# Kernel optimization log

Hardware: AMD Instinct MI355X
Metric: run time of the kernel (lower is better)

The kernel has to match this reference:

```python
import jax, jax.numpy as jnp
import numpy as np

L, D, H, B, SX, SY, VS, VT = 6, 1024, 16, 4, 512, 512, 32000, 32000
DK = D // H
FF = 4 * D
EPS = 1e-3          # LayerNorm eps (added to std, not var)
SCALE_EMB = float(np.sqrt(D))
NEG = -1e30         # stands in for -inf; fully-masked rows are zeroed after softmax


def pos_encoding(length, d):
    # tensor2tensor-style sinusoid: [sin | cos] concatenated along channels
    nt = d // 2
    lti = np.log(1e4) / (nt - 1)
    inv = np.exp(np.arange(nt) * -lti)
    st = np.arange(length)[:, None] * inv[None, :]
    return jnp.asarray(np.concatenate([np.sin(st), np.cos(st)], axis=1), jnp.float32)


def layer_norm(z, a, b):
    # faithful to the torch module: uses unbiased std (ddof=1) and divides by (std + eps)
    mu = z.mean(-1, keepdims=True)
    sig = jnp.sqrt(((z - mu) ** 2).sum(-1, keepdims=True) / (z.shape[-1] - 1))
    return (z - mu) / (sig + EPS) * a + b


def mha(xq, xkv, wq, wk, wv, wo, mask):
    # xq: (b, lq, D), xkv: (b, lk, D); head-chunking of channel dim == reshape to (H, DK)
    b, lq, _ = xq.shape
    q = (xq @ wq.T).reshape(b, lq, H, DK)
    k = (xkv @ wk.T).reshape(b, -1, H, DK)
    v = (xkv @ wv.T).reshape(b, -1, H, DK)
    s = jnp.einsum('bqhd,bkhd->bhqk', q, k) * (1.0 / np.sqrt(DK))
    m = mask[:, None, :, :]
    s = jnp.where(m, s, NEG)
    att = jax.nn.softmax(s, axis=-1)
    att = att * m.any(-1, keepdims=True)  # replicates NaN->0 for fully masked rows
    c = jnp.einsum('bhqk,bkhd->bqhd', att, v).reshape(b, lq, D)
    return c @ wo.T


def setup_inputs():
    key = jax.random.key(0)
    ks = jax.random.split(key, 10)
    s = 0.02
    emb_x = (jax.random.normal(ks[0], (VS, D), jnp.float32) * s).at[0].set(0.0)  # padding_idx=0
    emb_y = (jax.random.normal(ks[1], (VT, D), jnp.float32) * s).at[0].set(0.0)
    return {
        'emb_x': emb_x, 'emb_y': emb_y,
        'enc_qkvo': jax.random.normal(ks[2], (L, 4, D, D), jnp.float32) * s,
        'enc_ln_s': jnp.ones((L, 2, D), jnp.float32), 'enc_ln_b': jnp.zeros((L, 2, D), jnp.float32),
        'enc_w1': jax.random.normal(ks[3], (L, FF, D), jnp.float32) * s, 'enc_b1': jnp.zeros((L, FF), jnp.float32),
        'enc_w2': jax.random.normal(ks[4], (L, D, FF), jnp.float32) * s, 'enc_b2': jnp.zeros((L, D), jnp.float32),
        'dec_qkvo': jax.random.normal(ks[5], (L, 8, D, D), jnp.float32) * s,
        'dec_ln_s': jnp.ones((L, 3, D), jnp.float32), 'dec_ln_b': jnp.zeros((L, 3, D), jnp.float32),
        'dec_w1': jax.random.normal(ks[6], (L, FF, D), jnp.float32) * s, 'dec_b1': jnp.zeros((L, FF), jnp.float32),
        'dec_w2': jax.random.normal(ks[7], (L, D, FF), jnp.float32) * s, 'dec_b2': jnp.zeros((L, D), jnp.float32),
        'x_block': jax.random.randint(ks[8], (B, SX), 0, VS),
        'y_block': jax.random.randint(ks[9], (B, SY), 0, VT),
    }


def reference(emb_x, emb_y, enc_qkvo, enc_ln_s, enc_ln_b, enc_w1, enc_b1, enc_w2, enc_b2,
              dec_qkvo, dec_ln_s, dec_ln_b, dec_w1, dec_b1, dec_w2, dec_b2, x_block, y_block):
    # internal layout (b, len, D); torch code uses (b, D, len) -- math is identical
    ex = emb_x[x_block] * SCALE_EMB + pos_encoding(SX, D)[None]
    ey = emb_y[y_block] * SCALE_EMB + pos_encoding(SY, D)[None]
    xv = x_block != 0
    yv = y_block != 0
    xx = xv[:, :, None] & xv[:, None, :]                                   # (B, qx, kx)
    xy = yv[:, :, None] & xv[:, None, :]                                   # (B, qy, kx)
    yy = (yv[:, :, None] & yv[:, None, :]) & jnp.tril(jnp.ones((SY, SY), bool))[None]
    e = ex
    for i in range(L):
        sub = mha(e, e, enc_qkvo[i, 0], enc_qkvo[i, 1], enc_qkvo[i, 2], enc_qkvo[i, 3], xx)
        e = layer_norm(e + sub, enc_ln_s[i, 0], enc_ln_b[i, 0])
        sub = jax.nn.relu(e @ enc_w1[i].T + enc_b1[i]) @ enc_w2[i].T + enc_b2[i]
        e = layer_norm(e + sub, enc_ln_s[i, 1], enc_ln_b[i, 1])
    z = e
    e = ey
    for i in range(L):
        sub = mha(e, e, dec_qkvo[i, 0], dec_qkvo[i, 1], dec_qkvo[i, 2], dec_qkvo[i, 3], yy)
        e = layer_norm(e + sub, dec_ln_s[i, 0], dec_ln_b[i, 0])
        sub = mha(e, z, dec_qkvo[i, 4], dec_qkvo[i, 5], dec_qkvo[i, 6], dec_qkvo[i, 7], xy)
        e = layer_norm(e + sub, dec_ln_s[i, 1], dec_ln_b[i, 1])
        sub = jax.nn.relu(e @ dec_w1[i].T + dec_b1[i]) @ dec_w2[i].T + dec_b2[i]
        e = layer_norm(e + sub, dec_ln_s[i, 2], dec_ln_b[i, 2])
    return e @ emb_y.T  # tied output projection -> (B, SY, VT)
```

## Files before the change

### kernel.cpp

```cpp
#include <hip/hip_runtime.h>

typedef unsigned short u16;
typedef float f32x4 __attribute__((ext_vector_type(4)));
typedef __bf16 bf16x8 __attribute__((ext_vector_type(8)));
typedef u16 u16x8 __attribute__((ext_vector_type(8)));

#define DEV __device__ __forceinline__

DEV u16 f2bf(float f) {
  unsigned u = __builtin_bit_cast(unsigned, f);
  u += 0x7fffu + ((u >> 16) & 1u);
  return (u16)(u >> 16);
}

DEV float wsum(float v) {
#pragma unroll
  for (int o = 32; o > 0; o >>= 1) v += __shfl_xor(v, o, 64);
  return v;
}
DEV float gmax16(float v) {
#pragma unroll
  for (int o = 8; o > 0; o >>= 1) v = fmaxf(v, __shfl_xor(v, o, 64));
  return v;
}
DEV float gsum16(float v) {
#pragma unroll
  for (int o = 8; o > 0; o >>= 1) v += __shfl_xor(v, o, 64);
  return v;
}

DEV void gld16(const void* g, void* l) {
  __builtin_amdgcn_global_load_lds((const __attribute__((address_space(1))) void*)g,
                                   (__attribute__((address_space(3))) void*)l, 16, 0, 0);
}

template <int N>
DEV void vwait() {
  if constexpr (N == 0) asm volatile("s_waitcnt vmcnt(0)" ::: "memory");
  else if constexpr (N == 2) asm volatile("s_waitcnt vmcnt(2)" ::: "memory");
  else if constexpr (N == 4) asm volatile("s_waitcnt vmcnt(4)" ::: "memory");
  else asm volatile("s_waitcnt vmcnt(6)" ::: "memory");
}

DEV void remap_bxy(int& bx, int& by) {
  const int gx = gridDim.x, gy = gridDim.y;
  const int flat = blockIdx.y * gx + blockIdx.x;
  const int nwg = gx * gy;
  const int q = nwg >> 3, r = nwg & 7;
  const int xcd = flat & 7, li = flat >> 3;
  const int wg = (xcd < r ? xcd * (q + 1) : r * (q + 1) + (xcd - r) * q) + li;
  by = wg % gy;
  bx = wg / gy;
}

template <int BM, int BN, int MODE>
__global__ __launch_bounds__(256, 2) void gemm_k(
    const u16* __restrict__ A, const u16* __restrict__ B, int lda, int ldb, int K,
    float alpha, const float* __restrict__ bias, float* __restrict__ Cf, int ldc,
    u16* __restrict__ Cb, u16* __restrict__ qp, u16* __restrict__ kp,
    u16* __restrict__ vp, int n_off) {
  constexpr int FM = BM / 32, FN = BN / 32;
  constexpr int CHA = BM / 8, CHT = (BM + BN) / 8;
  __shared__ u16 lds[2][(BM + BN) * 64];
  const int lane = threadIdx.x & 63, wid = threadIdx.x >> 6;
  const int wr = wid >> 1, wc = wid & 1;
  int bx, by;
  remap_bxy(bx, by);
  const u16* gA = A + (long)(by * BM) * lda;
  const u16* gB = B + (long)(bx * BN) * ldb;

  const f32x4 zero4 = {0.f, 0.f, 0.f, 0.f};
  f32x4 acc[FM][FN];
#pragma unroll
  for (int m = 0; m < FM; ++m)
#pragma unroll
    for (int n = 0; n < FN; ++n) acc[m][n] = zero4;

  const int r8 = lane >> 3, sl = lane & 7;

  auto stage = [&](int buf, int kt) {
    const int kb = kt << 6;
#pragma unroll
    for (int c0 = 0; c0 < CHT; c0 += 4) {
      const int c = c0 + wid;
      u16* l = &lds[buf][c << 9];
      const u16* g;
      if (c < CHA) {
        int r = (c << 3) + r8;
        g = gA + (long)r * lda + kb + ((sl ^ (r & 7)) << 3);
      } else {
        int r = ((c - CHA) << 3) + r8;
        g = gB + (long)r * ldb + kb + ((sl ^ (r & 7)) << 3);
      }
      gld16(g, l);
    }
  };

  const int KT = K >> 6;
  stage(0, 0);
  __syncthreads();
  int cur = 0;
  for (int kt = 0; kt < KT; ++kt) {
    if (kt + 1 < KT) stage(cur ^ 1, kt + 1);
    const u16* lA = &lds[cur][0];
    const u16* lB = &lds[cur][BM << 6];
#pragma unroll
    for (int kk = 0; kk < 2; ++kk) {
      bf16x8 af[FM], bv[FN];
#pragma unroll
      for (int m = 0; m < FM; ++m) {
        int r = wr * (BM / 2) + m * 16 + (lane & 15);
        int slot = ((kk << 2) | (lane >> 4)) ^ (r & 7);
        af[m] = *(const bf16x8*)(lA + (r << 6) + (slot << 3));
      }
#pragma unroll
      for (int n = 0; n < FN; ++n) {
        int r = wc * (BN / 2) + n * 16 + (lane & 15);
        int slot = ((kk << 2) | (lane >> 4)) ^ (r & 7);
        bv[n] = *(const bf16x8*)(lB + (r << 6) + (slot << 3));
      }
#pragma unroll
      for (int m = 0; m < FM; ++m)
#pragma unroll
        for (int n = 0; n < FN; ++n)
          acc[m][n] = __builtin_amdgcn_mfma_f32_16x16x32_bf16(af[m], bv[n], acc[m][n], 0, 0, 0);
    }
    __syncthreads();
    cur ^= 1;
  }

  const int rb = by * BM + wr * (BM / 2) + ((lane >> 4) << 2);
  const int cb = bx * BN + wc * (BN / 2) + (lane & 15);
  if constexpr (MODE == 2) {
    const bool isV = (bx * BN + n_off) >= 2048;
    if (isV) {
      __syncthreads();
      u16* T = (u16*)&lds[0][0];
      constexpr int TS = BM + 8;
#pragma unroll
      for (int m = 0; m < FM; ++m)
#pragma unroll
        for (int n = 0; n < FN; ++n) {
          int cl = wc * (BN / 2) + n * 16 + (lane & 15);
#pragma unroll
          for (int j = 0; j < 4; ++j) {
            int rl = wr * (BM / 2) + m * 16 + ((lane >> 4) << 2) + j;
            T[cl * TS + rl] = f2bf(acc[m][n][j]);
          }
        }
      __syncthreads();
      const int vcb = bx * BN + n_off - 2048;
      const int b = (by * BM) >> 9, s0 = (by * BM) & 511;
#pragma unroll
      for (int p = 0; p < BM * BN / 2048; ++p) {
        int idx = p * 2048 + threadIdx.x * 8;
        int dl = idx / BM, slx = idx & (BM - 1);
        u16x8 o;
#pragma unroll
        for (int e = 0; e < 8; ++e) o[e] = T[dl * TS + slx + e];
        int vc = vcb + dl;
        *(u16x8*)(vp + (((long)b * 16 + (vc >> 6)) * 64 + (vc & 63)) * 512 + s0 + slx) = o;
      }
    } else {
#pragma unroll
      for (int m = 0; m < FM; ++m)
#pragma unroll
        for (int n = 0; n < FN; ++n)
#pragma unroll
          for (int j = 0; j < 4; ++j) {
            const int row = rb + m * 16 + j;
            const int np = cb + n * 16 + n_off;
            const int sel = np >> 10, dim = np & 1023;
            long base = (((long)(row >> 9) * 16 + (dim >> 6)) * 512 + (row & 511)) * 64 + (dim & 63);
            u16 val = f2bf(acc[m][n][j]);
            if (sel == 0) qp[base] = val;
            else kp[base] = val;
          }
    }
  } else {
#pragma unroll
    for (int m = 0; m < FM; ++m)
#pragma unroll
      for (int n = 0; n < FN; ++n)
#pragma unroll
        for (int j = 0; j < 4; ++j) {
          const int row = rb + m * 16 + j;
          const int col = cb + n * 16;
          float v = acc[m][n][j];
          if constexpr (MODE == 0) {
            float r = v * alpha;
            if (bias) r += bias[col];
            Cf[(long)row * ldc + col] = r;
          } else {
            Cb[(long)row * ldc + col] = f2bf(fmaxf(v + bias[col], 0.f));
          }
        }
  }
}

__global__ __launch_bounds__(512, 1) void gemm256_k(
    const u16* __restrict__ A, const u16* __restrict__ B, int lda, int ldb, int K,
    float* __restrict__ Cf, int ldc) {
  __shared__ u16 As[2][256 * 64];
  __shared__ u16 Bs[2][256 * 64];
  const int lane = threadIdx.x & 63, wid = threadIdx.x >> 6;
  const int wr = wid >> 2, wc = wid & 3;
  int bx, by;
  remap_bxy(bx, by);
  const u16* gA = A + (long)(by * 256) * lda;
  const u16* gB = B + (long)(bx * 256) * ldb;

  const f32x4 z4 = {0.f, 0.f, 0.f, 0.f};
  f32x4 acc[8][4];
#pragma unroll
  for (int m = 0; m < 8; ++m)
#pragma unroll
    for (int n = 0; n < 4; ++n) acc[m][n] = z4;

  const int ssl = lane & 7;

  auto stageH = [&](int t, int h) {
    const int kb = t << 6;
    const int buf = t & 1;
    const bool isA = (h == 0) || (h == 3);
    u16* ldsb = isA ? &As[buf][0] : &Bs[buf][0];
    const u16* gsrc = isA ? gA : gB;
    const int ld = isA ? lda : ldb;
    const int rbase = (h >= 2) ? 128 : 0;
#pragma unroll
    for (int rr = 0; rr < 2; ++rr) {
      const int r0 = rbase + rr * 64 + (wid << 3);
      const int r = r0 + (lane >> 3);
      gld16(gsrc + (long)r * ld + kb + ((ssl ^ (r & 7)) << 3), ldsb + (r0 << 6));
    }
  };

  const int KT = K >> 6;
  stageH(0, 0);
  stageH(0, 1);
  stageH(0, 2);
  stageH(0, 3);

  for (int t = 0; t < KT; ++t) {
    const int buf = t & 1;
    const bool more = (t + 1 < KT);
    const u16* lA = &As[buf][0];
    const u16* lB = &Bs[buf][0];
    bf16x8 af[4][2], bvl[2][2], bvh[2][2];

    vwait<4>();
    __builtin_amdgcn_s_barrier();
    __builtin_amdgcn_sched_barrier(0);
#pragma unroll
    for (int m = 0; m < 4; ++m)
#pragma unroll
      for (int kk = 0; kk < 2; ++kk) {
        int r = wr * 64 + m * 16 + (lane & 15);
        int sg = ((kk << 2) | (lane >> 4)) ^ (r & 7);
        af[m][kk] = *(const bf16x8*)(lA + (r << 6) + (sg << 3));
      }
#pragma unroll
    for (int n = 0; n < 2; ++n)
#pragma unroll
      for (int kk = 0; kk < 2; ++kk) {
        int c = wc * 32 + n * 16 + (lane & 15);
        int sg = ((kk << 2) | (lane >> 4)) ^ (c & 7);
        bvl[n][kk] = *(const bf16x8*)(lB + (c << 6) + (sg << 3));
      }
    if (more) stageH(t + 1, 0);
    __builtin_amdgcn_s_setprio(1);
#pragma unroll
    for (int kk = 0; kk < 2; ++kk)
#pragma unroll
      for (int m = 0; m < 4; ++m)
#pragma unroll
        for (int n = 0; n < 2; ++n)
          acc[m][n] = __builtin_amdgcn_mfma_f32_16x16x32_bf16(af[m][kk], bvl[n][kk], acc[m][n], 0, 0, 0);
    __builtin_amdgcn_s_setprio(0);

    if (more) vwait<4>();
    else vwait<2>();
    __builtin_amdgcn_s_barrier();
    __builtin_amdgcn_sched_barrier(0);
#pragma unroll
    for (int n = 0; n < 2; ++n)
#pragma unroll
      for (int kk = 0; kk < 2; ++kk) {
        int c = 128 + wc * 32 + n * 16 + (lane & 15);
        int sg = ((kk << 2) | (lane >> 4)) ^ (c & 7);
        bvh[n][kk] = *(const bf16x8*)(lB + (c << 6) + (sg << 3));
      }
    if (more) stageH(t + 1, 1);
    __builtin_amdgcn_s_setprio(1);
#pragma unroll
    for (int kk = 0; kk < 2; ++kk)
#pragma unroll
      for (int m = 0; m < 4; ++m)
#pragma unroll
        for (int n = 0; n < 2; ++n)
          acc[m][2 + n] = __builtin_amdgcn_mfma_f32_16x16x32_bf16(af[m][kk], bvh[n][kk], acc[m][2 + n], 0, 0, 0);
    __builtin_amdgcn_s_setprio(0);

    if (more) vwait<4>();
    else vwait<0>();
    __builtin_amdgcn_s_barrier();
    __builtin_amdgcn_sched_barrier(0);
#pragma unroll
    for (int m = 0; m < 4; ++m)
#pragma unroll
      for (int kk = 0; kk < 2; ++kk) {
        int r = 128 + wr * 64 + m * 16 + (lane & 15);
        int sg = ((kk << 2) | (lane >> 4)) ^ (r & 7);
        af[m][kk] = *(const bf16x8*)(lA + (r << 6) + (sg << 3));
      }
    if (more) stageH(t + 1, 2);
    __builtin_amdgcn_s_setprio(1);
#pragma unroll
    for (int kk = 0; kk < 2; ++kk)
#pragma unroll
      for (int m = 0; m < 4; ++m)
#pragma unroll
        for (int n = 0; n < 2; ++n)
          acc[4 + m][2 + n] = __builtin_amdgcn_mfma_f32_16x16x32_bf16(af[m][kk], bvh[n][kk], acc[4 + m][2 + n], 0, 0, 0);
    __builtin_amdgcn_s_setprio(0);

    __builtin_amdgcn_s_barrier();
    __builtin_amdgcn_sched_barrier(0);
    if (more) stageH(t + 1, 3);
    __builtin_amdgcn_s_setprio(1);
#pragma unroll
    for (int kk = 0; kk < 2; ++kk)
#pragma unroll
      for (int m = 0; m < 4; ++m)
#pragma unroll
        for (int n = 0; n < 2; ++n)
          acc[4 + m][n] = __builtin_amdgcn_mfma_f32_16x16x32_bf16(af[m][kk], bvl[n][kk], acc[4 + m][n], 0, 0, 0);
    __builtin_amdgcn_s_setprio(0);
  }

  const int rb = by * 256 + wr * 64 + ((lane >> 4) << 2);
  const int cb = bx * 256 + wc * 32 + (lane & 15);
#pragma unroll
  for (int mi = 0; mi < 8; ++mi)
#pragma unroll
    for (int ni = 0; ni < 4; ++ni)
#pragma unroll
      for (int j = 0; j < 4; ++j) {
        int row = rb + (mi & 3) * 16 + ((mi >> 2) << 7) + j;
        int col = cb + (ni & 1) * 16 + ((ni >> 1) << 7);
        Cf[(long)row * ldc + col] = acc[mi][ni][j];
      }
}

template <int CAUSAL>
__global__ __launch_bounds__(256, 2) void fattn_k(
    const u16* __restrict__ Qg, const u16* __restrict__ Kg, const u16* __restrict__ Vtg,
    const int* __restrict__ qids, const int* __restrict__ kids, u16* __restrict__ ctx) {
  __shared__ u16 Qs[128 * 64];
  __shared__ u16 Ks[2][64 * 64];
  __shared__ u16 Vs[2][64 * 64];
  __shared__ u16 Ps[4][32 * 64];
  const int lane = threadIdx.x & 63, wid = threadIdx.x >> 6;
  const int qt = blockIdx.x, bh = blockIdx.y, b = bh >> 4, h = bh & 15;
  const int q0 = qt << 7;
  const u16* Qbase = Qg + ((long)bh * 512 + q0) * 64;
  const u16* Kbase = Kg + (long)bh * 512 * 64;
  const u16* Vbase = Vtg + (long)bh * 64 * 512;
  const int r8 = lane >> 3, sl = lane & 7;

#pragma unroll
  for (int c0 = 0; c0 < 16; c0 += 4) {
    int c = c0 + wid;
    int r = (c << 3) + r8;
    gld16(Qbase + (long)r * 64 + ((sl ^ (r & 7)) << 3), &Qs[c << 9]);
  }

  auto stageKV = [&](int buf, int kt) {
#pragma unroll
    for (int c0 = 0; c0 < 16; c0 += 4) {
      int c = c0 + wid;
      if (c < 8) {
        int r = (c << 3) + r8;
        gld16(Kbase + (long)(kt * 64 + r) * 64 + ((sl ^ (r & 7)) << 3), &Ks[buf][c << 9]);
      } else {
        int r = ((c - 8) << 3) + r8;
        gld16(Vbase + (long)r * 512 + kt * 64 + ((sl ^ (r & 7)) << 3), &Vs[buf][(c - 8) << 9]);
      }
    }
  };

  const int NKT = CAUSAL ? ((q0 >> 6) + 2) : 8;
  stageKV(0, 0);
  __syncthreads();

  const f32x4 z4 = {0.f, 0.f, 0.f, 0.f};
  f32x4 oacc[2][4];
  float mrun[2][4], lrun[2][4];
  bool qv[2][4];
#pragma unroll
  for (int m = 0; m < 2; ++m)
#pragma unroll
    for (int j = 0; j < 4; ++j) {
      mrun[m][j] = -3e38f;
      lrun[m][j] = 0.f;
      int qg = q0 + wid * 32 + m * 16 + ((lane >> 4) << 2) + j;
      qv[m][j] = qids[(b << 9) + qg] != 0;
#pragma unroll
      for (int nd = 0; nd < 4; ++nd) oacc[m][nd] = z4;
    }

  int cur = 0;
  for (int kt = 0; kt < NKT; ++kt) {
    if (kt + 1 < NKT) stageKV(cur ^ 1, kt + 1);
    f32x4 s[2][4];
#pragma unroll
    for (int m = 0; m < 2; ++m)
#pragma unroll
      for (int n = 0; n < 4; ++n) s[m][n] = z4;
    __builtin_amdgcn_s_setprio(1);
#pragma unroll
    for (int kk = 0; kk < 2; ++kk) {
      bf16x8 aq[2], bk[4];
#pragma unroll
      for (int m = 0; m < 2; ++m) {
        int r = wid * 32 + m * 16 + (lane & 15);
        int slot = ((kk << 2) | (lane >> 4)) ^ (r & 7);
        aq[m] = *(const bf16x8*)&Qs[(r << 6) + (slot << 3)];
      }
#pragma unroll
      for (int n = 0; n < 4; ++n) {
        int c = n * 16 + (lane & 15);
        int slot = ((kk << 2) | (lane >> 4)) ^ (c & 7);
        bk[n] = *(const bf16x8*)&Ks[cur][(c << 6) + (slot << 3)];
      }
#pragma unroll
      for (int m = 0; m < 2; ++m)
#pragma unroll
        for (int n = 0; n < 4; ++n)
          s[m][n] = __builtin_amdgcn_mfma_f32_16x16x32_bf16(aq[m], bk[n], s[m][n], 0, 0, 0);
    }
    __builtin_amdgcn_s_setprio(0);
    bool kvld[4];
#pragma unroll
    for (int n = 0; n < 4; ++n)
      kvld[n] = kids[(b << 9) + (kt << 6) + (n << 4) + (lane & 15)] != 0;
    float mx[2][4];
#pragma unroll
    for (int m = 0; m < 2; ++m)
#pragma unroll
      for (int j = 0; j < 4; ++j) {
        mx[m][j] = -3e38f;
        int qg = q0 + wid * 32 + m * 16 + ((lane >> 4) << 2) + j;
#pragma unroll
        for (int n = 0; n < 4; ++n) {
          int colg = (kt << 6) + (n << 4) + (lane & 15);
          bool ok = qv[m][j] && kvld[n] && (!CAUSAL || colg <= qg);
          float sv = ok ? s[m][n][j] * 0.125f : -3e38f;
          s[m][n][j] = sv;
          mx[m][j] = fmaxf(mx[m][j], sv);
        }
        mx[m][j] = gmax16(mx[m][j]);
      }
#pragma unroll
    for (int m = 0; m < 2; ++m)
#pragma unroll
      for (int j = 0; j < 4; ++j) {
        float mn = fmaxf(mrun[m][j], mx[m][j]);
        float f = __expf(mrun[m][j] - mn);
        mrun[m][j] = mn;
        float ps = 0.f;
#pragma unroll
        for (int n = 0; n < 4; ++n) {
          float sv = s[m][n][j];
          float p = (sv > -1e37f) ? __expf(sv - mn) : 0.f;
          s[m][n][j] = p;
          ps += p;
        }
        ps = gsum16(ps);
        lrun[m][j] = lrun[m][j] * f + ps;
#pragma unroll
        for (int nd = 0; nd < 4; ++nd) oacc[m][nd][j] *= f;
      }
#pragma unroll
    for (int m = 0; m < 2; ++m)
#pragma unroll
      for (int n = 0; n < 4; ++n)
#pragma unroll
        for (int j = 0; j < 4; ++j) {
          int rl = (m << 4) + ((lane >> 4) << 2) + j;
          int slot = ((n << 1) | ((lane >> 3) & 1)) ^ (rl & 7);
          Ps[wid][(rl << 6) + (slot << 3) + (lane & 7)] = f2bf(s[m][n][j]);
        }
    __builtin_amdgcn_s_setprio(1);
#pragma unroll
    for (int kk = 0; kk < 2; ++kk) {
      bf16x8 pa[2], vv[4];
#pragma unroll
      for (int m = 0; m < 2; ++m) {
        int r = (m << 4) + (lane & 15);
        int slot = ((kk << 2) | (lane >> 4)) ^ (r & 7);
        pa[m] = *(const bf16x8*)&Ps[wid][(r << 6) + (slot << 3)];
      }
#pragma unroll
      for (int nd = 0; nd < 4; ++nd) {
        int rv = (nd << 4) + (lane & 15);
        int slot = ((kk << 2) | (lane >> 4)) ^ (rv & 7);
        vv[nd] = *(const bf16x8*)&Vs[cur][(rv << 6) + (slot << 3)];
      }
#pragma unroll
      for (int m = 0; m < 2; ++m)
#pragma unroll
        for (int nd = 0; nd < 4; ++nd)
          oacc[m][nd] = __builtin_amdgcn_mfma_f32_16x16x32_bf16(pa[m], vv[nd], oacc[m][nd], 0, 0, 0);
    }
    __builtin_amdgcn_s_setprio(0);
    __syncthreads();
    cur ^= 1;
  }
#pragma unroll
  for (int m = 0; m < 2; ++m)
#pragma unroll
    for (int j = 0; j < 4; ++j) {
      float inv = (lrun[m][j] > 0.f) ? 1.0f / lrun[m][j] : 0.f;
      int qg = q0 + wid * 32 + m * 16 + ((lane >> 4) << 2) + j;
      long rowb = (((long)(b << 9) + qg) * 16 + h) * 64;
#pragma unroll
      for (int nd = 0; nd < 4; ++nd) {
        int d = (nd << 4) + (lane & 15);
        ctx[rowb + d] = f2bf(oacc[m][nd][j] * inv);
      }
    }
}

__global__ __launch_bounds__(256) void embed_k(const int* __restrict__ ids,
                                               const float* __restrict__ emb,
                                               float* __restrict__ xo, u16* __restrict__ bfo) {
  const int tok = blockIdx.x, t = threadIdx.x;
  const int s = tok & 511;
  const long id = ids[tok];
  const int d = t * 4;
  float4 ev = *(const float4*)(emb + id * 1024 + d);
  float o[4] = {ev.x * 32.f, ev.y * 32.f, ev.z * 32.f, ev.w * 32.f};
#pragma unroll
  for (int j = 0; j < 4; ++j) {
    int dd = d + j, di = dd & 511;
    float ang = (float)s * expf(-(float)di * 0.0180241494559220821f);
    o[j] += (dd < 512) ? sinf(ang) : cosf(ang);
  }
  *(float4*)(xo + (long)tok * 1024 + d) = make_float4(o[0], o[1], o[2], o[3]);
  ushort4 ob = {f2bf(o[0]), f2bf(o[1]), f2bf(o[2]), f2bf(o[3])};
  *(ushort4*)(bfo + (long)tok * 1024 + d) = ob;
}

__global__ __launch_bounds__(256) void ln_k(const float* __restrict__ x,
                                            const float* __restrict__ sub,
                                            const float* __restrict__ gam,
                                            const float* __restrict__ bet,
                                            float* __restrict__ xo, u16* __restrict__ bfo) {
  __shared__ float red[8];
  const int row = blockIdx.x, t = threadIdx.x;
  const float4 xv = *(const float4*)(x + (long)row * 1024 + t * 4);
  const float4 sv = *(const float4*)(sub + (long)row * 1024 + t * 4);
  float v0 = xv.x + sv.x, v1 = xv.y + sv.y, v2 = xv.z + sv.z, v3 = xv.w + sv.w;
  float sm = wsum(v0 + v1 + v2 + v3);
  if ((t & 63) == 0) red[t >> 6] = sm;
  __syncthreads();
  const float mu = (red[0] + red[1] + red[2] + red[3]) * (1.0f / 1024.0f);
  const float d0 = v0 - mu, d1 = v1 - mu, d2 = v2 - mu, d3 = v3 - mu;
  float ss = wsum(d0 * d0 + d1 * d1 + d2 * d2 + d3 * d3);
  if ((t & 63) == 0) red[4 + (t >> 6)] = ss;
  __syncthreads();
  const float sig = sqrtf((red[4] + red[5] + red[6] + red[7]) * (1.0f / 1023.0f));
  const float inv = 1.0f / (sig + 0.001f);
  const float4 g4 = *(const float4*)(gam + t * 4);
  const float4 b4 = *(const float4*)(bet + t * 4);
  const float o0 = d0 * inv * g4.x + b4.x, o1 = d1 * inv * g4.y + b4.y;
  const float o2 = d2 * inv * g4.z + b4.z, o3 = d3 * inv * g4.w + b4.w;
  *(float4*)(xo + (long)row * 1024 + t * 4) = make_float4(o0, o1, o2, o3);
  ushort4 ob = {f2bf(o0), f2bf(o1), f2bf(o2), f2bf(o3)};
  *(ushort4*)(bfo + (long)row * 1024 + t * 4) = ob;
}

__global__ void cvt_k(const float* __restrict__ src, u16* __restrict__ dst, int n4) {
  for (int i = blockIdx.x * 256 + threadIdx.x; i < n4; i += gridDim.x * 256) {
    float4 v = ((const float4*)src)[i];
    ushort4 o = {f2bf(v.x), f2bf(v.y), f2bf(v.z), f2bf(v.w)};
    ((ushort4*)dst)[i] = o;
  }
}

__global__ void cvt3_k(const float* __restrict__ s0, int n0, const float* __restrict__ s1,
                       int n1, const float* __restrict__ s2, int n2, u16* __restrict__ dst) {
  const int tot = n0 + n1 + n2;
  for (int i = blockIdx.x * 256 + threadIdx.x; i < tot; i += gridDim.x * 256) {
    const float* s;
    int j;
    if (i < n0) { s = s0; j = i; }
    else if (i < n0 + n1) { s = s1; j = i - n0; }
    else { s = s2; j = i - n0 - n1; }
    float4 v = ((const float4*)s)[j];
    ushort4 o = {f2bf(v.x), f2bf(v.y), f2bf(v.z), f2bf(v.w)};
    ((ushort4*)dst)[i] = o;
  }
}

extern "C" void kernel_launch(void* const* d_in, const int* in_sizes, int n_in, void* d_out,
                              int out_size, void* d_ws, size_t ws_size, hipStream_t stream) {
  (void)in_sizes; (void)n_in; (void)out_size;
  const float* emb_x = (const float*)d_in[0];
  const float* emb_y = (const float*)d_in[1];
  const float* enc_qkvo = (const float*)d_in[2];
  const float* enc_ln_s = (const float*)d_in[3];
  const float* enc_ln_b = (const float*)d_in[4];
  const float* enc_w1 = (const float*)d_in[5];
  const float* enc_b1 = (const float*)d_in[6];
  const float* enc_w2 = (const float*)d_in[7];
  const float* enc_b2 = (const float*)d_in[8];
  const float* dec_qkvo = (const float*)d_in[9];
  const float* dec_ln_s = (const float*)d_in[10];
  const float* dec_ln_b = (const float*)d_in[11];
  const float* dec_w1 = (const float*)d_in[12];
  const float* dec_b1 = (const float*)d_in[13];
  const float* dec_w2 = (const float*)d_in[14];
  const float* dec_b2 = (const float*)d_in[15];
  const int* x_block = (const int*)d_in[16];
  const int* y_block = (const int*)d_in[17];

  const long TOK = 2048, Dm = 1024, M1 = 1048576;
  char* p = (char*)d_ws;
  auto alloc = [&](long bytes) { char* r = p; p += (bytes + 255) & ~255L; return r; };
  float* e32 = (float*)alloc(TOK * Dm * 4);
  float* sub = (float*)alloc(TOK * Dm * 4);
  u16* ebf = (u16*)alloc(TOK * Dm * 2);
  u16* zbf = (u16*)alloc(TOK * Dm * 2);
  u16* qb = (u16*)alloc(TOK * Dm * 2);
  u16* kb = (u16*)alloc(TOK * Dm * 2);
  u16* vtb = (u16*)alloc(TOK * Dm * 2);
  u16* ctx = (u16*)alloc(TOK * Dm * 2);
  u16* hbuf = (u16*)alloc(TOK * 4096 * 2);
  u16* wbuf = (u16*)alloc(16L * M1 * 2);
  u16* embyb = (u16*)alloc(32000L * 1024 * 2);
  if ((size_t)(p - (char*)d_ws) > ws_size) return;

  auto gemmF = [&](const u16* A, const u16* Bw, int M, int N, int K, int lda, int ldb,
                   float alpha, const float* bias, float* C, int ldc) {
    if (N % 128 == 0 && N > 1024) {
      dim3 g(N / 128, M / 128);
      gemm_k<128, 128, 0><<<g, 256, 0, stream>>>(A, Bw, lda, ldb, K, alpha, bias, C, ldc,
                                                 nullptr, nullptr, nullptr, nullptr, 0);
    } else {
      dim3 g(N / 64, M / 128);
      gemm_k<128, 64, 0><<<g, 256, 0, stream>>>(A, Bw, lda, ldb, K, alpha, bias, C, ldc,
                                                nullptr, nullptr, nullptr, nullptr, 0);
    }
  };
  auto gemmRelu = [&](const u16* A, const u16* Bw, const float* bias, u16* C) {
    dim3 g(32, 16);
    gemm_k<128, 128, 1><<<g, 256, 0, stream>>>(A, Bw, 1024, 1024, 1024, 1.f, bias, nullptr,
                                               4096, C, nullptr, nullptr, nullptr, 0);
  };
  auto gemmQKV = [&](const u16* A, const u16* Bw, int N, int n_off) {
    if (N >= 2048) {
      dim3 g(N / 128, 16);
      gemm_k<128, 128, 2><<<g, 256, 0, stream>>>(A, Bw, 1024, 1024, 1024, 1.f, nullptr,
                                                 nullptr, 0, nullptr, qb, kb, vtb, n_off);
    } else {
      dim3 g(N / 64, 16);
      gemm_k<128, 64, 2><<<g, 256, 0, stream>>>(A, Bw, 1024, 1024, 1024, 1.f, nullptr,
                                                nullptr, 0, nullptr, qb, kb, vtb, n_off);
    }
  };
  auto attn = [&](const int* qids, const int* kids, int causal) {
    if (causal)
      fattn_k<1><<<dim3(4, 64), 256, 0, stream>>>(qb, kb, vtb, qids, kids, ctx);
    else
      fattn_k<0><<<dim3(4, 64), 256, 0, stream>>>(qb, kb, vtb, qids, kids, ctx);
  };
  auto lnorm = [&](const float* g, const float* b) {
    ln_k<<<2048, 256, 0, stream>>>(e32, sub, g, b, e32, ebf);
  };

  cvt_k<<<2048, 256, 0, stream>>>(emb_y, embyb, 32000 * 1024 / 4);

  embed_k<<<2048, 256, 0, stream>>>(x_block, emb_x, e32, ebf);
  for (int i = 0; i < 6; ++i) {
    cvt3_k<<<2048, 256, 0, stream>>>(enc_qkvo + (long)i * 4 * M1, (int)M1,
                                     enc_w1 + (long)i * 4 * M1, (int)M1,
                                     enc_w2 + (long)i * 4 * M1, (int)M1, wbuf);
    gemmQKV(ebf, wbuf, 3072, 0);
    attn(x_block, x_block, 0);
    gemmF(ctx, wbuf + 3L * M1, 2048, 1024, 1024, 1024, 1024, 1.f, nullptr, sub, 1024);
    lnorm(enc_ln_s + (i * 2 + 0) * 1024, enc_ln_b + (i * 2 + 0) * 1024);
    gemmRelu(ebf, wbuf + 4L * M1, enc_b1 + i * 4096, hbuf);
    gemmF(hbuf, wbuf + 8L * M1, 2048, 1024, 4096, 4096, 4096, 1.f, enc_b2 + i * 1024, sub, 1024);
    lnorm(enc_ln_s + (i * 2 + 1) * 1024, enc_ln_b + (i * 2 + 1) * 1024);
  }
  hipMemcpyAsync(zbf, ebf, TOK * Dm * 2, hipMemcpyDeviceToDevice, stream);

  embed_k<<<2048, 256, 0, stream>>>(y_block, emb_y, e32, ebf);
  for (int i = 0; i < 6; ++i) {
    cvt3_k<<<2048, 256, 0, stream>>>(dec_qkvo + (long)i * 8 * M1, (int)(2 * M1),
                                     dec_w1 + (long)i * 4 * M1, (int)M1,
                                     dec_w2 + (long)i * 4 * M1, (int)M1, wbuf);
    gemmQKV(ebf, wbuf, 3072, 0);
    attn(y_block, y_block, 1);
    gemmF(ctx, wbuf + 3L * M1, 2048, 1024, 1024, 1024, 1024, 1.f, nullptr, sub, 1024);
    lnorm(dec_ln_s + (i * 3 + 0) * 1024, dec_ln_b + (i * 3 + 0) * 1024);
    gemmQKV(ebf, wbuf + 4L * M1, 1024, 0);
    gemmQKV(zbf, wbuf + 5L * M1, 2048, 1024);
    attn(y_block, x_block, 0);
    gemmF(ctx, wbuf + 7L * M1, 2048, 1024, 1024, 1024, 1024, 1.f, nullptr, sub, 1024);
    lnorm(dec_ln_s + (i * 3 + 1) * 1024, dec_ln_b + (i * 3 + 1) * 1024);
    gemmRelu(ebf, wbuf + 8L * M1, dec_b1 + i * 4096, hbuf);
    gemmF(hbuf, wbuf + 12L * M1, 2048, 1024, 4096, 4096, 4096, 1.f, dec_b2 + i * 1024, sub, 1024);
    lnorm(dec_ln_s + (i * 3 + 2) * 1024, dec_ln_b + (i * 3 + 2) * 1024);
  }
  gemm256_k<<<dim3(125, 8), 512, 0, stream>>>(ebf, embyb, 1024, 1024, 1024,
                                              (float*)d_out, 32000);
}
```

Before: 2.563 ms.

## Deepen GEMM global-to-LDS prefetch to a rolling seven-quarter-tile pipeline

Reworks the 256x256 GEMM main loop so quarter-tile global-to-LDS loads are issued from a rolling counter, running up to seven quarters ahead instead of one full K-tile. The per-phase vmcnt waits become a single wait at the end of each K-step. Extra barriers and lgkmcnt waits guard the LDS reads before each MFMA phase. The aim is to hide more global memory latency behind MFMA work, at the cost of more barriers per iteration and more outstanding loads in flight.

```diff
diff --git a/kernel.cpp b/kernel.cpp
--- a/kernel.cpp
+++ b/kernel.cpp
@@ -37,9 +37,8 @@
 template <int N>
 DEV void vwait() {
   if constexpr (N == 0) asm volatile("s_waitcnt vmcnt(0)" ::: "memory");
-  else if constexpr (N == 2) asm volatile("s_waitcnt vmcnt(2)" ::: "memory");
-  else if constexpr (N == 4) asm volatile("s_waitcnt vmcnt(4)" ::: "memory");
-  else asm volatile("s_waitcnt vmcnt(6)" ::: "memory");
+  else if constexpr (N == 6) asm volatile("s_waitcnt vmcnt(6)" ::: "memory");
+  else asm volatile("s_waitcnt vmcnt(8)" ::: "memory");
 }
 
 DEV void remap_bxy(int& bx, int& by) {
@@ -219,14 +218,14 @@
 
   const int ssl = lane & 7;
 
-  auto stageH = [&](int t, int h) {
-    const int kb = t << 6;
-    const int buf = t & 1;
-    const bool isA = (h == 0) || (h == 3);
+  auto issueH = [&](int h) {
+    const int th = h >> 2, region = h & 3, buf = th & 1;
+    const bool isA = (region == 0) || (region == 3);
     u16* ldsb = isA ? &As[buf][0] : &Bs[buf][0];
     const u16* gsrc = isA ? gA : gB;
     const int ld = isA ? lda : ldb;
-    const int rbase = (h >= 2) ? 128 : 0;
+    const int rbase = (region >= 2) ? 128 : 0;
+    const int kb = th << 6;
 #pragma unroll
     for (int rr = 0; rr < 2; ++rr) {
       const int r0 = rbase + rr * 64 + (wid << 3);
@@ -236,21 +235,18 @@
   };
 
   const int KT = K >> 6;
-  stageH(0, 0);
-  stageH(0, 1);
-  stageH(0, 2);
-  stageH(0, 3);
+  const int NH = KT << 2;
+  for (int h = 0; h < 7; ++h) issueH(h);
+  int nh = 7;
+  vwait<6>();
+  __builtin_amdgcn_s_barrier();
 
   for (int t = 0; t < KT; ++t) {
     const int buf = t & 1;
-    const bool more = (t + 1 < KT);
     const u16* lA = &As[buf][0];
     const u16* lB = &Bs[buf][0];
     bf16x8 af[4][2], bvl[2][2], bvh[2][2];
 
-    vwait<4>();
-    __builtin_amdgcn_s_barrier();
-    __builtin_amdgcn_sched_barrier(0);
 #pragma unroll
     for (int m = 0; m < 4; ++m)
 #pragma unroll
@@ -267,7 +263,10 @@
         int sg = ((kk << 2) | (lane >> 4)) ^ (c & 7);
         bvl[n][kk] = *(const bf16x8*)(lB + (c << 6) + (sg << 3));
       }
-    if (more) stageH(t + 1, 0);
+    if (nh < NH) issueH(nh++);
+    __builtin_amdgcn_s_barrier();
+    asm volatile("s_waitcnt lgkmcnt(0)" ::: "memory");
+    __builtin_amdgcn_sched_barrier(0);
     __builtin_amdgcn_s_setprio(1);
 #pragma unroll
     for (int kk = 0; kk < 2; ++kk)
@@ -277,11 +276,8 @@
         for (int n = 0; n < 2; ++n)
           acc[m][n] = __builtin_amdgcn_mfma_f32_16x16x32_bf16(af[m][kk], bvl[n][kk], acc[m][n], 0, 0, 0);
     __builtin_amdgcn_s_setprio(0);
-
-    if (more) vwait<4>();
-    else vwait<2>();
     __builtin_amdgcn_s_barrier();
-    __builtin_amdgcn_sched_barrier(0);
+
 #pragma unroll
     for (int n = 0; n < 2; ++n)
 #pragma unroll
@@ -290,7 +286,10 @@
         int sg = ((kk << 2) | (lane >> 4)) ^ (c & 7);
         bvh[n][kk] = *(const bf16x8*)(lB + (c << 6) + (sg << 3));
       }
-    if (more) stageH(t + 1, 1);
+    if (nh < NH) issueH(nh++);
+    __builtin_amdgcn_s_barrier();
+    asm volatile("s_waitcnt lgkmcnt(0)" ::: "memory");
+    __builtin_amdgcn_sched_barrier(0);
     __builtin_amdgcn_s_setprio(1);
 #pragma unroll
     for (int kk = 0; kk < 2; ++kk)
@@ -300,11 +299,8 @@
         for (int n = 0; n < 2; ++n)
           acc[m][2 + n] = __builtin_amdgcn_mfma_f32_16x16x32_bf16(af[m][kk], bvh[n][kk], acc[m][2 + n], 0, 0, 0);
     __builtin_amdgcn_s_setprio(0);
-
-    if (more) vwait<4>();
-    else vwait<0>();
     __builtin_amdgcn_s_barrier();
-    __builtin_amdgcn_sched_barrier(0);
+
 #pragma unroll
     for (int m = 0; m < 4; ++m)
 #pragma unroll
@@ -313,7 +309,10 @@
         int sg = ((kk << 2) | (lane >> 4)) ^ (r & 7);
         af[m][kk] = *(const bf16x8*)(lA + (r << 6) + (sg << 3));
       }
-    if (more) stageH(t + 1, 2);
+    if (nh < NH) issueH(nh++);
+    __builtin_amdgcn_s_barrier();
+    asm volatile("s_waitcnt lgkmcnt(0)" ::: "memory");
+    __builtin_amdgcn_sched_barrier(0);
     __builtin_amdgcn_s_setprio(1);
 #pragma unroll
     for (int kk = 0; kk < 2; ++kk)
@@ -323,10 +322,10 @@
         for (int n = 0; n < 2; ++n)
           acc[4 + m][2 + n] = __builtin_amdgcn_mfma_f32_16x16x32_bf16(af[m][kk], bvh[n][kk], acc[4 + m][2 + n], 0, 0, 0);
     __builtin_amdgcn_s_setprio(0);
-
     __builtin_amdgcn_s_barrier();
-    __builtin_amdgcn_sched_barrier(0);
-    if (more) stageH(t + 1, 3);
+
+    if (nh < NH) issueH(nh++);
+    __builtin_amdgcn_s_barrier();
     __builtin_amdgcn_s_setprio(1);
 #pragma unroll
     for (int kk = 0; kk < 2; ++kk)
@@ -336,6 +335,9 @@
         for (int n = 0; n < 2; ++n)
           acc[4 + m][n] = __builtin_amdgcn_mfma_f32_16x16x32_bf16(af[m][kk], bvl[n][kk], acc[4 + m][n], 0, 0, 0);
     __builtin_amdgcn_s_setprio(0);
+    if (t + 2 < KT) vwait<6>();
+    else if (t + 2 == KT) vwait<0>();
+    __builtin_amdgcn_s_barrier();
   }
 
   const int rb = by * 256 + wr * 64 + ((lane >> 4) << 2);
```

New measurement: 2.578 ms. No clear change (+0.6%).
